# Kernel tuning notes

Hardware: AMD Instinct MI355X
Metric: run time of the kernel (lower is better)

## Reference

```python
import jax, jax.numpy as jnp
import numpy as np

# Dim order: [N, K, C, P, Q, R, S]; memory levels: [L0_Registers, L1_Accumulator, L2_Scratchpad, L3_DRAM]
# Tensor types: 0=Input(N,C,P,Q) 1=Weight(K,C,R,S) 2=Output(N,K,P,Q)
DIM_MASK = jnp.array([[1,0,1,1,1,0,0],
                      [0,1,1,0,0,1,1],
                      [1,1,0,1,1,0,0]], dtype=bool)
# reuse dims: Input->K, Weight->N,P,Q, Output->C,R,S
REUSE_MASK = jnp.array([[0,1,0,0,0,0,0],
                        [1,0,0,1,1,0,0],
                        [0,0,1,0,0,1,1]], dtype=bool)

BYTES = 4.0
CLK_MHZ = 1000.0
DRAM_BW_GB_S = 100.0
PE_MAC_EPA_PJ = 0.56
L0_REG_EPA_PJ = 0.18
L1_BASE_EPA_PJ = 0.52
L1_COEFF_PJ_KB = 0.01
L2_BASE_EPA_PJ = 1.2
L2_COEFF_PJ_KB = 0.002
AREA_PER_PE = 0.01
AREA_PER_KB = 0.005

G = 500000  # number of (unfused) layers / fusion groups


def setup_inputs() -> dict:
    key = jax.random.key(0)
    k1, k2 = jax.random.split(key)
    temporal = 1.0 + jax.random.uniform(k1, (G, 7, 4), dtype=jnp.float32)
    spatial = 1.0 + jax.random.uniform(k2, (G, 7, 4), dtype=jnp.float32)
    return {
        "temporal_factors": temporal,
        "spatial_factors": spatial,
        "num_pes": jnp.array([256.0], dtype=jnp.float32),
        "buffer_sizes_kb": jnp.array([1.0, 64.0, 512.0], dtype=jnp.float32),  # L0, L1, L2
    }


def _masked_prod(x, mask):
    # x: [G,7,L], mask: [3,7] -> [G,3,L] product over masked dims
    return jnp.prod(jnp.where(mask[None, :, :, None], x[:, None, :, :], 1.0), axis=2)


def reference(temporal_factors, spatial_factors, num_pes, buffer_sizes_kb):
    pe = num_pes[0]
    sq = jnp.sqrt(pe)

    cumTS = jnp.cumprod(temporal_factors * spatial_factors, axis=2)  # prefix prod over levels
    cumT = jnp.cumprod(temporal_factors, axis=2)
    sufT = jnp.flip(jnp.cumprod(jnp.flip(temporal_factors, 2), 2), 2)  # suffix prod over levels

    macs = jnp.prod(cumTS[:, :, -1], axis=1)  # [G] product of full dim sizes

    fp = _masked_prod(cumTS, DIM_MASK)      # [G,3,4] data footprint up to level l
    outer = _masked_prod(sufT, DIM_MASK)    # [G,3,4] outer iterations from level l up
    ru = _masked_prod(cumT, REUSE_MASK)     # [G,3,4] reuse factor up to level l

    # interfaces (upper->lower): L3->L2, L2->L1, L1->L0
    low = jnp.array([2, 1, 0])
    up = jnp.array([3, 2, 1])
    acc = (fp[:, :, low] * (outer[:, :, up] / (ru[:, :, low] + 1e-9)) * BYTES).sum(axis=1)  # [G,3]

    # latency
    onchip_bw = 2.0 * sq * BYTES * CLK_MHZ * 1e6 / 1e9
    bw = jnp.stack([jnp.full((), DRAM_BW_GB_S), onchip_bw, onchip_bw])  # upper level bw per interface
    mem_lat = acc / (bw[None, :] * 1e9 + 1e-9)
    comp_lat = macs / (pe * CLK_MHZ * 1e6 + 1e-9)
    total_latency = jnp.maximum(comp_lat, mem_lat.max(axis=1)).sum()

    # energy (per interface, keyed by lower level: L2, L1, L0)
    epa = jnp.stack([
        L2_BASE_EPA_PJ + L2_COEFF_PJ_KB * buffer_sizes_kb[2],
        L1_BASE_EPA_PJ + L1_COEFF_PJ_KB * (buffer_sizes_kb[1] / sq),
        jnp.full((), L0_REG_EPA_PJ),
    ])
    total_energy = (macs * PE_MAC_EPA_PJ).sum() + ((acc / 4.0) @ epa).sum()

    # buffer mismatch for buffer levels L0, L1, L2
    req_kb = fp[:, :, :3].sum(axis=1) * BYTES / 1024.0  # [G,3]
    deficit = jax.nn.relu(req_kb - buffer_sizes_kb[None, :])
    total_mismatch = (deficit ** 2).sum()

    area = pe * AREA_PER_PE + (buffer_sizes_kb * AREA_PER_KB).sum()
    return (total_latency, total_energy, area, total_mismatch)
```

## Files before the change

### kernel.cpp

```cpp
#include <hip/hip_runtime.h>
#include <hip/hip_bf16.h>


typedef const __attribute__((address_space(1))) void* gptr_t;
typedef __attribute__((address_space(3))) void* lptr_t;

#define BLK 256
#define NBK 512

__global__ __launch_bounds__(BLK) void hpm_main(
    const float* __restrict__ T, const float* __restrict__ S,
    const float* __restrict__ PE, const float* __restrict__ BUF,
    double* __restrict__ part, int G)
{
    __shared__ float ldsT[BLK * 28];
    __shared__ float ldsS[BLK * 28];

    const int tid = threadIdx.x;
    const int wid = tid >> 6;
    const int NT  = (G + BLK - 1) / BLK;

    const float pe = PE[0];
    const float sq = sqrtf(pe);
    const float b0 = BUF[0], b1 = BUF[1], b2 = BUF[2];
    const float bw_dram   = 100.0f * 1e9f + 1e-9f;
    const float bw_onchip = sq * 8e9f + 1e-9f;
    const float epa0 = 1.2f  + 0.002f * b2;
    const float epa1 = 0.52f + 0.01f  * (b1 / sq);
    const float epa2 = 0.18f;
    const float inv_pe = 1.0f / (pe * 1e9f + 1e-9f);

    auto issue_dma = [&](int t) {
        const float* gT = T + (size_t)t * BLK * 28;
        const float* gS = S + (size_t)t * BLK * 28;
        #pragma unroll
        for (int k = 0; k < 7; ++k) {
            const int fidx = k * BLK + tid;
            const int uoff = (k * BLK + wid * 64) * 4;
            __builtin_amdgcn_global_load_lds((gptr_t)(gT + (size_t)fidx * 4),
                                             (lptr_t)&ldsT[uoff], 16, 0, 0);
            __builtin_amdgcn_global_load_lds((gptr_t)(gS + (size_t)fidx * 4),
                                             (lptr_t)&ldsS[uoff], 16, 0, 0);
        }
    };

    double latA = 0.0, enA = 0.0, misA = 0.0;

    {
        const int t0 = blockIdx.x;
        if (t0 < NT && t0 * BLK + BLK <= G) issue_dma(t0);
    }

    for (int t = blockIdx.x; t < NT; t += NBK) {
        const bool full = (t * BLK + BLK <= G);
        const int  g    = t * BLK + tid;

        float4 tv[7], sv[7];
        bool have = false;

        __syncthreads();

        if (full) {
            const float4* Tl = reinterpret_cast<const float4*>(&ldsT[tid * 28]);
            const float4* Sl = reinterpret_cast<const float4*>(&ldsS[tid * 28]);
            #pragma unroll
            for (int d = 0; d < 7; ++d) { tv[d] = Tl[d]; sv[d] = Sl[d]; }
            have = true;
        } else if (g < G) {
            const float4* Tp = reinterpret_cast<const float4*>(T) + (size_t)g * 7;
            const float4* Sp = reinterpret_cast<const float4*>(S) + (size_t)g * 7;
            #pragma unroll
            for (int d = 0; d < 7; ++d) { tv[d] = Tp[d]; sv[d] = Sp[d]; }
            have = true;
        }

        __syncthreads();

        {
            const int tn = t + NBK;
            if (tn < NT && tn * BLK + BLK <= G) issue_dma(tn);
        }

        if (have) {
            float fpI[3] = {1.f,1.f,1.f}, fpW[3] = {1.f,1.f,1.f}, fpO[3] = {1.f,1.f,1.f};
            float otI[3] = {1.f,1.f,1.f}, otW[3] = {1.f,1.f,1.f}, otO[3] = {1.f,1.f,1.f};
            float ruI[3] = {1.f,1.f,1.f}, ruW[3] = {1.f,1.f,1.f}, ruO[3] = {1.f,1.f,1.f};
            float macs = 1.f;

            constexpr unsigned IN_D = 0x1D, WT_D = 0x66, OU_D = 0x1B;
            constexpr unsigned IN_R = 0x02, WT_R = 0x19, OU_R = 0x64;

            #pragma unroll
            for (int d = 0; d < 7; ++d) {
                const float4 tt = tv[d];
                const float4 ss = sv[d];

                const float ct0 = tt.x;
                const float ct1 = ct0 * tt.y;
                const float ct2 = ct1 * tt.z;
                const float u0 = tt.x * ss.x, u1 = tt.y * ss.y;
                const float u2 = tt.z * ss.z, u3 = tt.w * ss.w;
                const float cs0 = u0;
                const float cs1 = cs0 * u1;
                const float cs2 = cs1 * u2;
                const float cs3 = cs2 * u3;
                const float st3 = tt.w;
                const float st2 = tt.z * st3;
                const float st1 = tt.y * st2;

                macs *= cs3;

                if ((IN_D >> d) & 1) {
                    fpI[0] *= cs0; fpI[1] *= cs1; fpI[2] *= cs2;
                    otI[0] *= st1; otI[1] *= st2; otI[2] *= st3;
                }
                if ((WT_D >> d) & 1) {
                    fpW[0] *= cs0; fpW[1] *= cs1; fpW[2] *= cs2;
                    otW[0] *= st1; otW[1] *= st2; otW[2] *= st3;
                }
                if ((OU_D >> d) & 1) {
                    fpO[0] *= cs0; fpO[1] *= cs1; fpO[2] *= cs2;
                    otO[0] *= st1; otO[1] *= st2; otO[2] *= st3;
                }
                if ((IN_R >> d) & 1) { ruI[0] *= ct0; ruI[1] *= ct1; ruI[2] *= ct2; }
                if ((WT_R >> d) & 1) { ruW[0] *= ct0; ruW[1] *= ct1; ruW[2] *= ct2; }
                if ((OU_R >> d) & 1) { ruO[0] *= ct0; ruO[1] *= ct1; ruO[2] *= ct2; }
            }

            const float acc0 = 4.f * ( fpI[2] * otI[2] / (ruI[2] + 1e-9f)
                                     + fpW[2] * otW[2] / (ruW[2] + 1e-9f)
                                     + fpO[2] * otO[2] / (ruO[2] + 1e-9f) );
            const float acc1 = 4.f * ( fpI[1] * otI[1] / (ruI[1] + 1e-9f)
                                     + fpW[1] * otW[1] / (ruW[1] + 1e-9f)
                                     + fpO[1] * otO[1] / (ruO[1] + 1e-9f) );
            const float acc2 = 4.f * ( fpI[0] * otI[0] / (ruI[0] + 1e-9f)
                                     + fpW[0] * otW[0] / (ruW[0] + 1e-9f)
                                     + fpO[0] * otO[0] / (ruO[0] + 1e-9f) );

            const float ml = fmaxf(acc0 / bw_dram, fmaxf(acc1, acc2) / bw_onchip);
            const float cl = macs * inv_pe;
            latA += (double)fmaxf(cl, ml);

            enA += (double)(macs * 0.56f + (acc0 * epa0 + acc1 * epa1 + acc2 * epa2) * 0.25f);

            const float c = 4.f / 1024.f;
            const float r0 = (fpI[0] + fpW[0] + fpO[0]) * c;
            const float r1 = (fpI[1] + fpW[1] + fpO[1]) * c;
            const float r2 = (fpI[2] + fpW[2] + fpO[2]) * c;
            const float d0 = fmaxf(r0 - b0, 0.f);
            const float d1 = fmaxf(r1 - b1, 0.f);
            const float d2 = fmaxf(r2 - b2, 0.f);
            misA += (double)d0 * d0 + (double)d1 * d1 + (double)d2 * d2;
        }
    }

    #pragma unroll
    for (int off = 32; off > 0; off >>= 1) {
        latA += __shfl_down(latA, off);
        enA  += __shfl_down(enA,  off);
        misA += __shfl_down(misA, off);
    }

    __shared__ double sred[3][4];
    const int lane = tid & 63;
    if (lane == 0) { sred[0][wid] = latA; sred[1][wid] = enA; sred[2][wid] = misA; }
    __syncthreads();

    if (tid == 0) {
        double L = 0.0, E = 0.0, M = 0.0;
        #pragma unroll
        for (int w = 0; w < 4; ++w) { L += sred[0][w]; E += sred[1][w]; M += sred[2][w]; }
        part[0 * NBK + blockIdx.x] = L;
        part[1 * NBK + blockIdx.x] = E;
        part[2 * NBK + blockIdx.x] = M;
    }
}

__global__ __launch_bounds__(256) void hpm_final(
    const double* __restrict__ part,
    const float* __restrict__ PE, const float* __restrict__ BUF,
    float* __restrict__ out)
{
    const int tid = threadIdx.x;
    double L = 0.0, E = 0.0, M = 0.0;
    #pragma unroll
    for (int i = tid; i < NBK; i += 256) {
        L += part[0 * NBK + i];
        E += part[1 * NBK + i];
        M += part[2 * NBK + i];
    }

    #pragma unroll
    for (int off = 32; off > 0; off >>= 1) {
        L += __shfl_down(L, off);
        E += __shfl_down(E, off);
        M += __shfl_down(M, off);
    }

    __shared__ double sred[3][4];
    const int wid  = tid >> 6;
    const int lane = tid & 63;
    if (lane == 0) { sred[0][wid] = L; sred[1][wid] = E; sred[2][wid] = M; }
    __syncthreads();

    if (tid == 0) {
        double Lt = 0.0, Et = 0.0, Mt = 0.0;
        #pragma unroll
        for (int w = 0; w < 4; ++w) { Lt += sred[0][w]; Et += sred[1][w]; Mt += sred[2][w]; }
        out[0] = (float)Lt;
        out[1] = (float)Et;
        out[2] = PE[0] * 0.01f + (BUF[0] + BUF[1] + BUF[2]) * 0.005f;
        out[3] = (float)Mt;
    }
}

extern "C" void kernel_launch(void* const* d_in, const int* in_sizes, int n_in,
                              void* d_out, int out_size, void* d_ws, size_t ws_size,
                              hipStream_t stream) {
    const float* T   = (const float*)d_in[0];
    const float* S   = (const float*)d_in[1];
    const float* PE  = (const float*)d_in[2];
    const float* BUF = (const float*)d_in[3];
    float* out = (float*)d_out;
    double* ws = (double*)d_ws;

    const int G = in_sizes[0] / 28;

    hipLaunchKernelGGL(hpm_main, dim3(NBK), dim3(BLK), 0, stream,
                       T, S, PE, BUF, ws, G);
    hipLaunchKernelGGL(hpm_final, dim3(1), dim3(256), 0, stream,
                       ws, PE, BUF, out);
}
```

Baseline: 26.52 us.

## Double-buffer LDS async loads with explicit vmcnt waits and halve grid size

Adds a second LDS buffer so global-to-LDS loads for tile i+2 run while tile i is computed. Explicit s_waitcnt vmcnt(14) waits replace the __syncthreads pair. The grid drops from 512 to 256 blocks, and block 0 handles the partial tail tile. LDS per block doubles, which may lower occupancy, and the hard-coded vmcnt count relies on exactly 14 loads per issue.

```diff
diff --git a/kernel.cpp b/kernel.cpp
--- a/kernel.cpp
+++ b/kernel.cpp
@@ -6,19 +6,21 @@
 typedef __attribute__((address_space(3))) void* lptr_t;
 
 #define BLK 256
-#define NBK 512
+#define NBK 256
 
 __global__ __launch_bounds__(BLK) void hpm_main(
     const float* __restrict__ T, const float* __restrict__ S,
     const float* __restrict__ PE, const float* __restrict__ BUF,
     double* __restrict__ part, int G)
 {
-    __shared__ float ldsT[BLK * 28];
-    __shared__ float ldsS[BLK * 28];
+    __shared__ float ldsT[2][BLK * 28];
+    __shared__ float ldsS[2][BLK * 28];
 
     const int tid = threadIdx.x;
     const int wid = tid >> 6;
-    const int NT  = (G + BLK - 1) / BLK;
+    const int NTF = G / BLK;
+    const int b   = blockIdx.x;
+    const int cnt = (NTF > b) ? ((NTF - 1 - b) / NBK + 1) : 0;
 
     const float pe = PE[0];
     const float sq = sqrtf(pe);
@@ -30,7 +32,10 @@
     const float epa2 = 0.18f;
     const float inv_pe = 1.0f / (pe * 1e9f + 1e-9f);
 
-    auto issue_dma = [&](int t) {
+    constexpr unsigned IN_D = 0x1D, WT_D = 0x66, OU_D = 0x1B;
+    constexpr unsigned IN_R = 0x02, WT_R = 0x19, OU_R = 0x64;
+
+    auto issue = [&](int t, int buf) {
         const float* gT = T + (size_t)t * BLK * 28;
         const float* gS = S + (size_t)t * BLK * 28;
         #pragma unroll
@@ -38,119 +43,120 @@
             const int fidx = k * BLK + tid;
             const int uoff = (k * BLK + wid * 64) * 4;
             __builtin_amdgcn_global_load_lds((gptr_t)(gT + (size_t)fidx * 4),
-                                             (lptr_t)&ldsT[uoff], 16, 0, 0);
+                                             (lptr_t)&ldsT[buf][uoff], 16, 0, 0);
             __builtin_amdgcn_global_load_lds((gptr_t)(gS + (size_t)fidx * 4),
-                                             (lptr_t)&ldsS[uoff], 16, 0, 0);
+                                             (lptr_t)&ldsS[buf][uoff], 16, 0, 0);
         }
     };
 
     double latA = 0.0, enA = 0.0, misA = 0.0;
 
-    {
-        const int t0 = blockIdx.x;
-        if (t0 < NT && t0 * BLK + BLK <= G) issue_dma(t0);
-    }
-
-    for (int t = blockIdx.x; t < NT; t += NBK) {
-        const bool full = (t * BLK + BLK <= G);
-        const int  g    = t * BLK + tid;
-
+    auto accumulate = [&](const float4* tv, const float4* sv) {
+        float fpI[3] = {1.f,1.f,1.f}, fpW[3] = {1.f,1.f,1.f}, fpO[3] = {1.f,1.f,1.f};
+        float otI[3] = {1.f,1.f,1.f}, otW[3] = {1.f,1.f,1.f}, otO[3] = {1.f,1.f,1.f};
+        float ruI[3] = {1.f,1.f,1.f}, ruW[3] = {1.f,1.f,1.f}, ruO[3] = {1.f,1.f,1.f};
+        float macs = 1.f;
+
+        #pragma unroll
+        for (int d = 0; d < 7; ++d) {
+            const float4 tt = tv[d];
+            const float4 ss = sv[d];
+
+            const float ct0 = tt.x;
+            const float ct1 = ct0 * tt.y;
+            const float ct2 = ct1 * tt.z;
+            const float u0 = tt.x * ss.x, u1 = tt.y * ss.y;
+            const float u2 = tt.z * ss.z, u3 = tt.w * ss.w;
+            const float cs0 = u0;
+            const float cs1 = cs0 * u1;
+            const float cs2 = cs1 * u2;
+            const float cs3 = cs2 * u3;
+            const float st3 = tt.w;
+            const float st2 = tt.z * st3;
+            const float st1 = tt.y * st2;
+
+            macs *= cs3;
+
+            if ((IN_D >> d) & 1) {
+                fpI[0] *= cs0; fpI[1] *= cs1; fpI[2] *= cs2;
+                otI[0] *= st1; otI[1] *= st2; otI[2] *= st3;
+            }
+            if ((WT_D >> d) & 1) {
+                fpW[0] *= cs0; fpW[1] *= cs1; fpW[2] *= cs2;
+                otW[0] *= st1; otW[1] *= st2; otW[2] *= st3;
+            }
+            if ((OU_D >> d) & 1) {
+                fpO[0] *= cs0; fpO[1] *= cs1; fpO[2] *= cs2;
+                otO[0] *= st1; otO[1] *= st2; otO[2] *= st3;
+            }
+            if ((IN_R >> d) & 1) { ruI[0] *= ct0; ruI[1] *= ct1; ruI[2] *= ct2; }
+            if ((WT_R >> d) & 1) { ruW[0] *= ct0; ruW[1] *= ct1; ruW[2] *= ct2; }
+            if ((OU_R >> d) & 1) { ruO[0] *= ct0; ruO[1] *= ct1; ruO[2] *= ct2; }
+        }
+
+        const float acc0 = 4.f * ( fpI[2] * otI[2] / (ruI[2] + 1e-9f)
+                                 + fpW[2] * otW[2] / (ruW[2] + 1e-9f)
+                                 + fpO[2] * otO[2] / (ruO[2] + 1e-9f) );
+        const float acc1 = 4.f * ( fpI[1] * otI[1] / (ruI[1] + 1e-9f)
+                                 + fpW[1] * otW[1] / (ruW[1] + 1e-9f)
+                                 + fpO[1] * otO[1] / (ruO[1] + 1e-9f) );
+        const float acc2 = 4.f * ( fpI[0] * otI[0] / (ruI[0] + 1e-9f)
+                                 + fpW[0] * otW[0] / (ruW[0] + 1e-9f)
+                                 + fpO[0] * otO[0] / (ruO[0] + 1e-9f) );
+
+        const float ml = fmaxf(acc0 / bw_dram, fmaxf(acc1, acc2) / bw_onchip);
+        const float cl = macs * inv_pe;
+        latA += (double)fmaxf(cl, ml);
+
+        enA += (double)(macs * 0.56f + (acc0 * epa0 + acc1 * epa1 + acc2 * epa2) * 0.25f);
+
+        const float c = 4.f / 1024.f;
+        const float r0 = (fpI[0] + fpW[0] + fpO[0]) * c;
+        const float r1 = (fpI[1] + fpW[1] + fpO[1]) * c;
+        const float r2 = (fpI[2] + fpW[2] + fpO[2]) * c;
+        const float d0 = fmaxf(r0 - b0, 0.f);
+        const float d1 = fmaxf(r1 - b1, 0.f);
+        const float d2 = fmaxf(r2 - b2, 0.f);
+        misA += (double)d0 * d0 + (double)d1 * d1 + (double)d2 * d2;
+    };
+
+    if (cnt > 0) issue(b, 0);
+    if (cnt > 1) issue(b + NBK, 1);
+
+    for (int i = 0; i < cnt; ++i) {
+        if (i + 1 < cnt) { asm volatile("s_waitcnt vmcnt(14)" ::: "memory"); }
+        else             { asm volatile("s_waitcnt vmcnt(0)"  ::: "memory"); }
+        __builtin_amdgcn_sched_barrier(0);
+        __builtin_amdgcn_s_barrier();
+        __builtin_amdgcn_sched_barrier(0);
+
+        const int buf = i & 1;
         float4 tv[7], sv[7];
-        bool have = false;
-
-        __syncthreads();
-
-        if (full) {
-            const float4* Tl = reinterpret_cast<const float4*>(&ldsT[tid * 28]);
-            const float4* Sl = reinterpret_cast<const float4*>(&ldsS[tid * 28]);
+        {
+            const float4* Tl = reinterpret_cast<const float4*>(&ldsT[buf][tid * 28]);
+            const float4* Sl = reinterpret_cast<const float4*>(&ldsS[buf][tid * 28]);
             #pragma unroll
             for (int d = 0; d < 7; ++d) { tv[d] = Tl[d]; sv[d] = Sl[d]; }
-            have = true;
-        } else if (g < G) {
+        }
+        asm volatile("s_waitcnt lgkmcnt(0)" ::: "memory");
+        __builtin_amdgcn_sched_barrier(0);
+        __builtin_amdgcn_s_barrier();
+        __builtin_amdgcn_sched_barrier(0);
+
+        if (i + 2 < cnt) issue(b + (size_t)(i + 2) * NBK, buf);
+
+        accumulate(tv, sv);
+    }
+
+    if (b == 0) {
+        const int g = NTF * BLK + tid;
+        if (g < G) {
+            float4 tv[7], sv[7];
             const float4* Tp = reinterpret_cast<const float4*>(T) + (size_t)g * 7;
             const float4* Sp = reinterpret_cast<const float4*>(S) + (size_t)g * 7;
             #pragma unroll
             for (int d = 0; d < 7; ++d) { tv[d] = Tp[d]; sv[d] = Sp[d]; }
-            have = true;
-        }
-
-        __syncthreads();
-
-        {
-            const int tn = t + NBK;
-            if (tn < NT && tn * BLK + BLK <= G) issue_dma(tn);
-        }
-
-        if (have) {
-            float fpI[3] = {1.f,1.f,1.f}, fpW[3] = {1.f,1.f,1.f}, fpO[3] = {1.f,1.f,1.f};
-            float otI[3] = {1.f,1.f,1.f}, otW[3] = {1.f,1.f,1.f}, otO[3] = {1.f,1.f,1.f};
-            float ruI[3] = {1.f,1.f,1.f}, ruW[3] = {1.f,1.f,1.f}, ruO[3] = {1.f,1.f,1.f};
-            float macs = 1.f;
-
-            constexpr unsigned IN_D = 0x1D, WT_D = 0x66, OU_D = 0x1B;
-            constexpr unsigned IN_R = 0x02, WT_R = 0x19, OU_R = 0x64;
-
-            #pragma unroll
-            for (int d = 0; d < 7; ++d) {
-                const float4 tt = tv[d];
-                const float4 ss = sv[d];
-
-                const float ct0 = tt.x;
-                const float ct1 = ct0 * tt.y;
-                const float ct2 = ct1 * tt.z;
-                const float u0 = tt.x * ss.x, u1 = tt.y * ss.y;
-                const float u2 = tt.z * ss.z, u3 = tt.w * ss.w;
-                const float cs0 = u0;
-                const float cs1 = cs0 * u1;
-                const float cs2 = cs1 * u2;
-                const float cs3 = cs2 * u3;
-                const float st3 = tt.w;
-                const float st2 = tt.z * st3;
-                const float st1 = tt.y * st2;
-
-                macs *= cs3;
-
-                if ((IN_D >> d) & 1) {
-                    fpI[0] *= cs0; fpI[1] *= cs1; fpI[2] *= cs2;
-                    otI[0] *= st1; otI[1] *= st2; otI[2] *= st3;
-                }
-                if ((WT_D >> d) & 1) {
-                    fpW[0] *= cs0; fpW[1] *= cs1; fpW[2] *= cs2;
-                    otW[0] *= st1; otW[1] *= st2; otW[2] *= st3;
-                }
-                if ((OU_D >> d) & 1) {
-                    fpO[0] *= cs0; fpO[1] *= cs1; fpO[2] *= cs2;
-                    otO[0] *= st1; otO[1] *= st2; otO[2] *= st3;
-                }
-                if ((IN_R >> d) & 1) { ruI[0] *= ct0; ruI[1] *= ct1; ruI[2] *= ct2; }
-                if ((WT_R >> d) & 1) { ruW[0] *= ct0; ruW[1] *= ct1; ruW[2] *= ct2; }
-                if ((OU_R >> d) & 1) { ruO[0] *= ct0; ruO[1] *= ct1; ruO[2] *= ct2; }
-            }
-
-            const float acc0 = 4.f * ( fpI[2] * otI[2] / (ruI[2] + 1e-9f)
-                                     + fpW[2] * otW[2] / (ruW[2] + 1e-9f)
-                                     + fpO[2] * otO[2] / (ruO[2] + 1e-9f) );
-            const float acc1 = 4.f * ( fpI[1] * otI[1] / (ruI[1] + 1e-9f)
-                                     + fpW[1] * otW[1] / (ruW[1] + 1e-9f)
-                                     + fpO[1] * otO[1] / (ruO[1] + 1e-9f) );
-            const float acc2 = 4.f * ( fpI[0] * otI[0] / (ruI[0] + 1e-9f)
-                                     + fpW[0] * otW[0] / (ruW[0] + 1e-9f)
-                                     + fpO[0] * otO[0] / (ruO[0] + 1e-9f) );
-
-            const float ml = fmaxf(acc0 / bw_dram, fmaxf(acc1, acc2) / bw_onchip);
-            const float cl = macs * inv_pe;
-            latA += (double)fmaxf(cl, ml);
-
-            enA += (double)(macs * 0.56f + (acc0 * epa0 + acc1 * epa1 + acc2 * epa2) * 0.25f);
-
-            const float c = 4.f / 1024.f;
-            const float r0 = (fpI[0] + fpW[0] + fpO[0]) * c;
-            const float r1 = (fpI[1] + fpW[1] + fpO[1]) * c;
-            const float r2 = (fpI[2] + fpW[2] + fpO[2]) * c;
-            const float d0 = fmaxf(r0 - b0, 0.f);
-            const float d1 = fmaxf(r1 - b1, 0.f);
-            const float d2 = fmaxf(r2 - b2, 0.f);
-            misA += (double)d0 * d0 + (double)d1 * d1 + (double)d2 * d2;
+            accumulate(tv, sv);
         }
     }
 
@@ -183,11 +189,10 @@
 {
     const int tid = threadIdx.x;
     double L = 0.0, E = 0.0, M = 0.0;
-    #pragma unroll
-    for (int i = tid; i < NBK; i += 256) {
-        L += part[0 * NBK + i];
-        E += part[1 * NBK + i];
-        M += part[2 * NBK + i];
+    if (tid < NBK) {
+        L = part[0 * NBK + tid];
+        E = part[1 * NBK + tid];
+        M = part[2 * NBK + tid];
     }
 
     #pragma unroll
```

Measured after the change: 26.25 us. No clear change (-1.0%).
